# Kernel optimization log

Hardware: AMD Instinct MI355X
Metric: run time of the kernel (lower is better)

Reference implementation:

```python
import jax, jax.numpy as jnp
import numpy as np

N, E, L, H, C, F_IN = 50000, 800000, 3, 8, 16, 128  # nodes, edges, layers, heads, per-head dim, input dim
NEG_SLOPE = 0.2


def setup_inputs() -> dict:
    key = jax.random.key(0)
    k = jax.random.split(key, 8)
    scale = 0.1
    x = jax.random.normal(k[0], (N, F_IN), dtype=jnp.float32)
    Ws = jax.random.normal(k[1], (L, F_IN, H * C), dtype=jnp.float32) * scale
    att_src = jax.random.normal(k[2], (L, H, C), dtype=jnp.float32) * scale
    att_dst = jax.random.normal(k[3], (L, H, C), dtype=jnp.float32) * scale
    biases = jnp.zeros((L, H * C), dtype=jnp.float32)
    fc_w = jax.random.normal(k[4], (H * C, C), dtype=jnp.float32) * scale
    fc_b = jnp.zeros((C,), dtype=jnp.float32)
    edge_index = jax.random.randint(k[5], (2, E), 0, N, dtype=jnp.int64)
    return {"x": x, "Ws": Ws, "att_src": att_src, "att_dst": att_dst,
            "biases": biases, "fc_w": fc_w, "fc_b": fc_b, "edge_index": edge_index}


def _gat_layer(x, W, a_src, a_dst, b, src, dst):
    # x: [N, F]; W: [F, H*C]; a_src/a_dst: [H, C]; src/dst: [E+N] (self-loops included)
    n = x.shape[0]
    h = (x @ W).reshape(n, H, C)                      # [N, H, C]
    e_src = jnp.einsum('nhc,hc->nh', h, a_src)        # [N, H]
    e_dst = jnp.einsum('nhc,hc->nh', h, a_dst)
    e = jax.nn.leaky_relu(e_src[src] + e_dst[dst], NEG_SLOPE)   # [E+N, H]
    # segment softmax over incoming edges of each target node
    emax = jax.ops.segment_max(e, dst, num_segments=n)          # [N, H]
    ex = jnp.exp(e - emax[dst])
    denom = jax.ops.segment_sum(ex, dst, num_segments=n)        # [N, H]
    alpha = ex / (denom[dst] + 1e-16)                            # [E+N, H]
    out = jax.ops.segment_sum(alpha[:, :, None] * h[src], dst, num_segments=n)  # [N, H, C]
    return out.reshape(n, H * C) + b


def reference(x, Ws, att_src, att_dst, biases, fc_w, fc_b, edge_index):
    loop = jnp.arange(N, dtype=edge_index.dtype)
    src = jnp.concatenate([edge_index[0], loop])  # add self-loops (PyG default)
    dst = jnp.concatenate([edge_index[1], loop])
    h = x
    for l in range(L):
        h = _gat_layer(h, Ws[l], att_src[l], att_dst[l], biases[l], src, dst)
        h = jax.nn.elu(h)
    return h @ fc_w + fc_b  # [N, C]
```

## Files before the change

kernel.cpp:

```cpp
#include <hip/hip_runtime.h>
#include <hip/hip_bf16.h>


#define GAT_F 128
#define GAT_H 8
#define GAT_C 16

typedef __attribute__((ext_vector_type(8))) short bf16x8;
typedef __attribute__((ext_vector_type(4))) float f32x4;

__device__ __forceinline__ float bf2f(unsigned short u) {
    union { unsigned int i; float f; } x; x.i = ((unsigned int)u) << 16; return x.f;
}
__device__ __forceinline__ float bfhi2f(unsigned int u) {
    union { unsigned int i; float f; } x; x.i = u & 0xFFFF0000u; return x.f;
}
__device__ __forceinline__ float bflo2f(unsigned int u) {
    union { unsigned int i; float f; } x; x.i = u << 16; return x.f;
}
__device__ __forceinline__ unsigned int pk_bf16(float a, float b) {
    union { float f; unsigned int i; } ua, ub;
    ua.f = a; ub.f = b;
    unsigned int ra = (ua.i + 0x7FFFu + ((ua.i >> 16) & 1u)) >> 16;
    unsigned int rb = (ub.i + 0x7FFFu + ((ub.i >> 16) & 1u)) & 0xFFFF0000u;
    return ra | rb;
}
__device__ __forceinline__ unsigned short f2bf(float a) {
    union { float f; unsigned int i; } ua; ua.f = a;
    return (unsigned short)((ua.i + 0x7FFFu + ((ua.i >> 16) & 1u)) >> 16);
}
__device__ __forceinline__ float ldf(const void* p, size_t i, int isf32) {
    return isf32 ? ((const float*)p)[i] : bf2f(((const unsigned short*)p)[i]);
}
__device__ __forceinline__ int ldei(const int* ei, int i, int is64) {
    return is64 ? ei[2 * (size_t)i] : ei[i];
}

__global__ void k_detect(const unsigned short* __restrict__ xb,
                         const int* __restrict__ ei, int* flags) {
    __shared__ int nan_cnt, zero_cnt;
    if (threadIdx.x == 0) { nan_cnt = 0; zero_cnt = 0; }
    __syncthreads();
    int t = threadIdx.x;
    int ln = 0;
    for (int i = t; i < 8192; i += 256) {
        unsigned short u = xb[i];
        if ((u & 0x7F80) == 0x7F80) ln++;
    }
    int lz = 0;
    for (int i = t; i < 2048; i += 256) {
        if (ei[2 * i + 1] == 0) lz++;
    }
    if (ln) atomicAdd(&nan_cnt, ln);
    if (lz) atomicAdd(&zero_cnt, lz);
    __syncthreads();
    if (t == 0) {
        flags[0] = (nan_cnt > 3) ? 1 : 0;
        flags[1] = (zero_cnt > 1024) ? 1 : 0;
    }
}

__global__ void k_prep(const void* __restrict__ W, const void* __restrict__ asrc,
                       const void* __restrict__ adst,
                       unsigned short* __restrict__ wt, unsigned short* __restrict__ wa,
                       int Lw, const int* __restrict__ flags) {
    int isf32 = flags[0];
    int b = blockIdx.x, t = threadIdx.x;
    if (b < Lw * 64) {
        int gid = b * 256 + t;
        int l = gid >> 14, r = gid & 16383;
        int c = r >> 7, k = r & 127;
        float v = ldf(W, (size_t)l * 16384 + k * 128 + c, isf32);
        wt[gid] = f2bf(v);
    } else {
        int id = (b - Lw * 64) * 256 + t;
        int l = id >> 11, q = id & 2047;
        int j = q >> 7, k = q & 127;
        int head = j & 7;
        const void* av = (j < 8) ? asrc : adst;
        float acc = 0.f;
        #pragma unroll
        for (int cc = 0; cc < 16; cc++) {
            float w = ldf(W, (size_t)l * 16384 + k * 128 + head * 16 + cc, isf32);
            float a = ldf(av, (size_t)l * 128 + head * 16 + cc, isf32);
            acc += w * a;
        }
        wa[id] = f2bf(acc);
    }
}

__global__ void k_init_deg(int* deg, int n) {
    int i = blockIdx.x * 256 + threadIdx.x;
    if (i < n) deg[i] = 1;
}

__global__ void k_count_deg(const int* __restrict__ ei, int* deg, int E,
                            const int* __restrict__ flags) {
    int k = blockIdx.x * 256 + threadIdx.x;
    int is64 = flags[1];
    if (k < E) atomicAdd(&deg[ldei(ei, E + k, is64)], 1);
}

__global__ __launch_bounds__(256) void k_scan_blk(
    const int* __restrict__ deg, int* __restrict__ rp_local,
    int* __restrict__ bsum, int n)
{
    int b = blockIdx.x, t = threadIdx.x;
    int i0 = b * 1024 + t * 4;
    int v0 = 0, v1 = 0, v2 = 0, v3 = 0;
    if (i0 + 3 < n) {
        int4 d = *(const int4*)(deg + i0);
        v0 = d.x; v1 = d.y; v2 = d.z; v3 = d.w;
    } else {
        if (i0     < n) v0 = deg[i0];
        if (i0 + 1 < n) v1 = deg[i0 + 1];
        if (i0 + 2 < n) v2 = deg[i0 + 2];
        if (i0 + 3 < n) v3 = deg[i0 + 3];
    }
    int s = v0 + v1 + v2 + v3;
    int lane = t & 63, wid = t >> 6;
    int sc = s;
    #pragma unroll
    for (int off = 1; off < 64; off <<= 1) {
        int o = __shfl_up(sc, off);
        if (lane >= off) sc += o;
    }
    __shared__ int wsum[4];
    if (lane == 63) wsum[wid] = sc;
    __syncthreads();
    int woff = 0;
    #pragma unroll
    for (int w2 = 0; w2 < 4; w2++) if (w2 < wid) woff += wsum[w2];
    int excl = woff + sc - s;
    if (i0     < n) rp_local[i0]     = excl;
    if (i0 + 1 < n) rp_local[i0 + 1] = excl + v0;
    if (i0 + 2 < n) rp_local[i0 + 2] = excl + v0 + v1;
    if (i0 + 3 < n) rp_local[i0 + 3] = excl + v0 + v1 + v2;
    if (t == 255) bsum[b] = woff + sc;
}

__global__ __launch_bounds__(256) void k_scan_top(
    int* __restrict__ bsum, int* __restrict__ rowptr, int nb, int n)
{
    __shared__ int sh[1024];
    int t = threadIdx.x;
    for (int i = t; i < 1024; i += 256) sh[i] = (i < nb) ? bsum[i] : 0;
    __syncthreads();
    for (int off = 1; off < 1024; off <<= 1) {
        int vals[4];
        #pragma unroll
        for (int k = 0; k < 4; k++) {
            int i = t + 256 * k;
            vals[k] = (i >= off) ? sh[i - off] : 0;
        }
        __syncthreads();
        #pragma unroll
        for (int k = 0; k < 4; k++) sh[t + 256 * k] += vals[k];
        __syncthreads();
    }
    for (int i = t; i < nb; i += 256) bsum[i] = (i == 0) ? 0 : sh[i - 1];
    if (t == 0) rowptr[n] = sh[nb - 1];
}

__global__ void k_place_add(int* __restrict__ rowptr, const int* __restrict__ bsum,
                            int* __restrict__ adj, int* __restrict__ cursor, int n)
{
    int i = blockIdx.x * 256 + threadIdx.x;
    if (i < n) {
        int r = rowptr[i] + bsum[i >> 10];
        rowptr[i] = r;
        adj[r] = i;
        cursor[i] = 1;
    }
    if (blockIdx.x == 0 && threadIdx.x < 8) adj[rowptr[n] + threadIdx.x] = 0;
}

__global__ void k_scatter(const int* __restrict__ ei, const int* __restrict__ rowptr,
                          int* __restrict__ cursor, int* __restrict__ adj, int E,
                          const int* __restrict__ flags) {
    int k = blockIdx.x * 256 + threadIdx.x;
    int is64 = flags[1];
    if (k < E) {
        int s = ldei(ei, k, is64);
        int d = ldei(ei, E + k, is64);
        int p = atomicAdd(&cursor[d], 1);
        adj[rowptr[d] + p] = s;
    }
}

__global__ __launch_bounds__(256) void k_gemm_mfma(
    const void* __restrict__ xin, int x_is_input,
    const unsigned short* __restrict__ wt,
    const unsigned short* __restrict__ wa,
    unsigned int* __restrict__ hb, float* __restrict__ es, float* __restrict__ ed,
    int n, const int* __restrict__ flags)
{
    __shared__ unsigned short xl[64 * 136];
    __shared__ unsigned short wl[144 * 136];
    int isf32 = flags[0];
    int t = threadIdx.x;
    int row0 = blockIdx.x * 64;

    if (isf32 || !x_is_input) {
        const float4* xg = (const float4*)xin;
        for (int i = t; i < 2048; i += 256) {
            int r = i >> 5, c4 = i & 31;
            int gr = row0 + r;
            uint2 u = make_uint2(0u, 0u);
            if (gr < n) {
                float4 v = xg[(size_t)gr * 32 + c4];
                u = make_uint2(pk_bf16(v.x, v.y), pk_bf16(v.z, v.w));
            }
            *(uint2*)&xl[r * 136 + c4 * 4] = u;
        }
    } else {
        const ushort4* xg = (const ushort4*)xin;
        for (int i = t; i < 2048; i += 256) {
            int r = i >> 5, c4 = i & 31;
            int gr = row0 + r;
            ushort4 v = make_ushort4(0, 0, 0, 0);
            if (gr < n) v = xg[(size_t)gr * 32 + c4];
            *(ushort4*)&xl[r * 136 + c4 * 4] = v;
        }
    }
    {
        const ushort4* wg = (const ushort4*)wt;
        for (int i = t; i < 4096; i += 256) {
            int c = i >> 5, k4 = i & 31;
            *(ushort4*)&wl[c * 136 + k4 * 4] = wg[i];
        }
        const ushort4* wag = (const ushort4*)wa;
        for (int i = t; i < 512; i += 256) {
            int j = i >> 5, k4 = i & 31;
            *(ushort4*)&wl[(128 + j) * 136 + k4 * 4] = wag[i];
        }
    }
    __syncthreads();

    int lane = t & 63, wid = t >> 6, quad = lane >> 4, col = lane & 15;
    f32x4 acc[9];
    #pragma unroll
    for (int ct = 0; ct < 9; ct++) acc[ct] = (f32x4){0.f, 0.f, 0.f, 0.f};

    #pragma unroll
    for (int ks = 0; ks < 4; ks++) {
        int k0 = ks * 32;
        bf16x8 af = *(const bf16x8*)&xl[(wid * 16 + col) * 136 + k0 + quad * 8];
        #pragma unroll
        for (int ct = 0; ct < 9; ct++) {
            bf16x8 bf = *(const bf16x8*)&wl[(ct * 16 + col) * 136 + k0 + quad * 8];
            acc[ct] = __builtin_amdgcn_mfma_f32_16x16x32_bf16(af, bf, acc[ct], 0, 0, 0);
        }
    }

    #pragma unroll
    for (int ct = 0; ct < 8; ct++) {
        #pragma unroll
        for (int r = 0; r < 4; r++) {
            int grow = row0 + wid * 16 + quad * 4 + r;
            float v = acc[ct][r];
            float vp = __shfl_xor(v, 1);
            if (!(lane & 1) && grow < n)
                hb[(size_t)grow * 64 + ct * 8 + (col >> 1)] = pk_bf16(v, vp);
        }
    }
    #pragma unroll
    for (int r = 0; r < 4; r++) {
        int grow = row0 + wid * 16 + quad * 4 + r;
        float v = acc[8][r];
        if (grow < n) {
            if (col < 8) es[(size_t)grow * 8 + col] = v;
            else         ed[(size_t)grow * 8 + col - 8] = v;
        }
    }
}

__global__ __launch_bounds__(256) void k_aggregate(
    const unsigned int* __restrict__ hb,
    const float* __restrict__ es, const float* __restrict__ ed,
    const int* __restrict__ rowptr, const int* __restrict__ adj,
    const void* __restrict__ bias, long b_off, float* __restrict__ out, int n,
    const int* __restrict__ flags)
{
    __shared__ __align__(16) float alds[4][64 * 12];
    __shared__ __align__(16) int   slds[4][64];
    int isf32 = flags[0];
    int lane = threadIdx.x & 63;
    int wid = threadIdx.x >> 6;
    int node = blockIdx.x * 4 + wid;
    if (node >= n) return;
    int base = rowptr[node];
    int deg = rowptr[node + 1] - base;
    int head = lane >> 3;

    const float4* es4 = (const float4*)es;
    const float4* ed4 = (const float4*)ed;
    float edv[8];
    {
        float4 a = ed4[node * 2];
        float4 b = ed4[node * 2 + 1];
        edv[0] = a.x; edv[1] = a.y; edv[2] = a.z; edv[3] = a.w;
        edv[4] = b.x; edv[5] = b.y; edv[6] = b.z; edv[7] = b.w;
    }

    float acc0 = 0.f, acc1 = 0.f, lsum = 0.f;
    for (int j0 = 0; j0 < deg; j0 += 64) {
        int j = j0 + lane;
        int sp = (j < deg) ? adj[base + j] : 0;
        float4 ea = es4[sp * 2];
        float4 eb = es4[sp * 2 + 1];
        float ev[8] = {ea.x, ea.y, ea.z, ea.w, eb.x, eb.y, eb.z, eb.w};
        float p[8];
        #pragma unroll
        for (int hh = 0; hh < 8; hh++) {
            float v = ev[hh] + edv[hh];
            v = fmaxf(v, 0.2f * v);
            float pe = __expf(v);
            p[hh] = (j < deg) ? pe : 0.f;
        }
        *(float4*)&alds[wid][lane * 12]     = make_float4(p[0], p[1], p[2], p[3]);
        *(float4*)&alds[wid][lane * 12 + 4] = make_float4(p[4], p[5], p[6], p[7]);
        slds[wid][lane] = sp;
        __builtin_amdgcn_s_waitcnt(0);

        int lim = min(64, deg - j0);
        for (int jj = 0; jj < lim; jj += 4) {
            int4 sv = *(const int4*)&slds[wid][jj];
            float a0 = alds[wid][(jj + 0) * 12 + head];
            float a1 = alds[wid][(jj + 1) * 12 + head];
            float a2 = alds[wid][(jj + 2) * 12 + head];
            float a3 = alds[wid][(jj + 3) * 12 + head];
            unsigned int h0 = hb[sv.x * 64 + lane];
            unsigned int h1 = hb[sv.y * 64 + lane];
            unsigned int h2 = hb[sv.z * 64 + lane];
            unsigned int h3 = hb[sv.w * 64 + lane];
            lsum += (a0 + a1) + (a2 + a3);
            acc0 += a0 * bflo2f(h0) + a1 * bflo2f(h1) + a2 * bflo2f(h2) + a3 * bflo2f(h3);
            acc1 += a0 * bfhi2f(h0) + a1 * bfhi2f(h1) + a2 * bfhi2f(h2) + a3 * bfhi2f(h3);
        }
    }

    float inv = 1.f / (lsum + 1e-16f);
    int ch = lane << 1;
    float o0 = acc0 * inv + ldf(bias, b_off + ch, isf32);
    float o1 = acc1 * inv + ldf(bias, b_off + ch + 1, isf32);
    o0 = o0 > 0.f ? o0 : (__expf(o0) - 1.f);
    o1 = o1 > 0.f ? o1 : (__expf(o1) - 1.f);
    *(float2*)(out + (size_t)node * GAT_F + ch) = make_float2(o0, o1);
}

__global__ __launch_bounds__(256) void k_fc(
    const float* __restrict__ h, const void* __restrict__ fw,
    const void* __restrict__ fb, void* __restrict__ out, int n,
    const int* __restrict__ flags)
{
    __shared__ float fws[GAT_F * GAT_C];
    int isf32 = flags[0];
    int t = threadIdx.x;
    for (int i = t; i < GAT_F * GAT_C; i += 256)
        fws[i] = ldf(fw, i, isf32);
    __syncthreads();
    int row = blockIdx.x * 256 + t;
    if (row >= n) return;
    float acc[16];
    #pragma unroll
    for (int c = 0; c < 16; c++) acc[c] = ldf(fb, c, isf32);
    const float4* hr = (const float4*)(h + (size_t)row * GAT_F);
    for (int k4 = 0; k4 < GAT_F / 4; k4++) {
        float4 xv = hr[k4];
        float xs4[4] = {xv.x, xv.y, xv.z, xv.w};
        #pragma unroll
        for (int kk = 0; kk < 4; kk++) {
            int k = k4 * 4 + kk;
            const float4* wr = (const float4*)(fws + k * GAT_C);
            #pragma unroll
            for (int c4 = 0; c4 < 4; c4++) {
                float4 wv = wr[c4];
                acc[c4 * 4 + 0] += xs4[kk] * wv.x;
                acc[c4 * 4 + 1] += xs4[kk] * wv.y;
                acc[c4 * 4 + 2] += xs4[kk] * wv.z;
                acc[c4 * 4 + 3] += xs4[kk] * wv.w;
            }
        }
    }
    if (isf32) {
        float* o = (float*)out + (size_t)row * GAT_C;
        #pragma unroll
        for (int c = 0; c < 16; c++) o[c] = acc[c];
    } else {
        __hip_bfloat16* o = (__hip_bfloat16*)out + (size_t)row * GAT_C;
        #pragma unroll
        for (int c = 0; c < 16; c++) o[c] = __float2bfloat16(acc[c]);
    }
}

extern "C" void kernel_launch(void* const* d_in, const int* in_sizes, int n_in,
                              void* d_out, int out_size, void* d_ws, size_t ws_size,
                              hipStream_t stream) {
    const void* x      = d_in[0];
    const void* Ws     = d_in[1];
    const void* att_s  = d_in[2];
    const void* att_d  = d_in[3];
    const void* biases = d_in[4];
    const void* fc_w   = d_in[5];
    const void* fc_b   = d_in[6];
    const int*  ei     = (const int*)d_in[7];

    const int N  = in_sizes[0] / GAT_F;
    const int E  = in_sizes[7] / 2;
    const int L  = in_sizes[1] / (GAT_F * GAT_F);
    const int ET = E + N;

    char* w = (char*)d_ws;
    int* flags         = (int*)w;            w += 64;
    float* hA          = (float*)w;          w += (size_t)N * GAT_F * 4;
    unsigned int* hB   = (unsigned int*)w;   w += (size_t)N * 64 * 4;
    float* es          = (float*)w;          w += (size_t)N * GAT_H * 4;
    float* ed          = (float*)w;          w += (size_t)N * GAT_H * 4;
    int* rowptr        = (int*)w;            w += (((size_t)(N + 1) * 4 + 15) & ~15ull);
    int* cursor        = (int*)w;            w += (size_t)N * 4;
    int* bsum          = (int*)w;            w += 1024 * 4;
    int* adj           = (int*)w;            w += (size_t)(ET + 16) * 4;
    unsigned short* wt = (unsigned short*)w; w += (size_t)L * 16384 * 2;
    unsigned short* wa = (unsigned short*)w; w += (size_t)L * 2048 * 2;

    int nb_n = (N + 255) / 256;
    int nb_e = (E + 255) / 256;
    int nb_s = (N + 1023) / 1024;

    k_detect<<<1, 256, 0, stream>>>((const unsigned short*)x, ei, flags);
    k_prep<<<L * 64 + L * 8, 256, 0, stream>>>(Ws, att_s, att_d, wt, wa, L, flags);

    k_init_deg<<<nb_n, 256, 0, stream>>>(cursor, N);
    k_count_deg<<<nb_e, 256, 0, stream>>>(ei, cursor, E, flags);
    k_scan_blk<<<nb_s, 256, 0, stream>>>(cursor, rowptr, bsum, N);
    k_scan_top<<<1, 256, 0, stream>>>(bsum, rowptr, nb_s, N);
    k_place_add<<<nb_n, 256, 0, stream>>>(rowptr, bsum, adj, cursor, N);
    k_scatter<<<nb_e, 256, 0, stream>>>(ei, rowptr, cursor, adj, E, flags);

    int nb_g = (N + 63) / 64;
    int nb_a = (N + 3) / 4;
    for (int l = 0; l < L; l++) {
        k_gemm_mfma<<<nb_g, 256, 0, stream>>>(
            (l == 0) ? x : (const void*)hA, (l == 0) ? 1 : 0,
            wt + (size_t)l * 16384, wa + (size_t)l * 2048,
            hB, es, ed, N, flags);
        k_aggregate<<<nb_a, 256, 0, stream>>>(
            hB, es, ed, rowptr, adj,
            biases, (long)l * GAT_F, hA, N, flags);
    }
    k_fc<<<nb_n, 256, 0, stream>>>(hA, fc_w, fc_b, d_out, N, flags);
}
```

Before: 400.6 us.

## Store hidden activations as bf16, read GEMM operands directly, unroll aggregation by eight

Intermediate layer outputs are now packed bf16 instead of fp32, which halves the write traffic in aggregate and the read traffic in the following GEMM and FC kernels. The GEMM no longer stages weights in LDS and reads bf16 activations straight from global memory, keeping LDS staging only for the fp32 input. Aggregation gathers eight neighbours per iteration, with padded zero slots and a relaxed waitcnt. Edge count and scatter kernels handle two edges per thread with vector loads. The extra bf16 rounding between layers reduces precision, and the uncached global loads of the B operand may cost more than LDS reads.

```diff
diff --git a/kernel.cpp b/kernel.cpp
--- a/kernel.cpp
+++ b/kernel.cpp
@@ -96,9 +96,17 @@
 
 __global__ void k_count_deg(const int* __restrict__ ei, int* deg, int E,
                             const int* __restrict__ flags) {
-    int k = blockIdx.x * 256 + threadIdx.x;
+    int k2 = (blockIdx.x * 256 + threadIdx.x) * 2;
     int is64 = flags[1];
-    if (k < E) atomicAdd(&deg[ldei(ei, E + k, is64)], 1);
+    if (k2 + 1 < E) {
+        int d0, d1;
+        if (is64) { int4 v = *(const int4*)&ei[2 * (size_t)(E + k2)]; d0 = v.x; d1 = v.z; }
+        else      { int2 v = *(const int2*)&ei[E + k2]; d0 = v.x; d1 = v.y; }
+        atomicAdd(&deg[d0], 1);
+        atomicAdd(&deg[d1], 1);
+    } else if (k2 < E) {
+        atomicAdd(&deg[ldei(ei, E + k2, is64)], 1);
+    }
 }
 
 __global__ __launch_bounds__(256) void k_scan_blk(
@@ -178,11 +186,24 @@
 __global__ void k_scatter(const int* __restrict__ ei, const int* __restrict__ rowptr,
                           int* __restrict__ cursor, int* __restrict__ adj, int E,
                           const int* __restrict__ flags) {
-    int k = blockIdx.x * 256 + threadIdx.x;
+    int k2 = (blockIdx.x * 256 + threadIdx.x) * 2;
     int is64 = flags[1];
-    if (k < E) {
-        int s = ldei(ei, k, is64);
-        int d = ldei(ei, E + k, is64);
+    if (k2 + 1 < E) {
+        int s0, s1, d0, d1;
+        if (is64) {
+            int4 a = *(const int4*)&ei[2 * (size_t)k2];       s0 = a.x; s1 = a.z;
+            int4 b = *(const int4*)&ei[2 * (size_t)(E + k2)]; d0 = b.x; d1 = b.z;
+        } else {
+            int2 a = *(const int2*)&ei[k2];     s0 = a.x; s1 = a.y;
+            int2 b = *(const int2*)&ei[E + k2]; d0 = b.x; d1 = b.y;
+        }
+        int p0 = atomicAdd(&cursor[d0], 1);
+        adj[rowptr[d0] + p0] = s0;
+        int p1 = atomicAdd(&cursor[d1], 1);
+        adj[rowptr[d1] + p1] = s1;
+    } else if (k2 < E) {
+        int s = ldei(ei, k2, is64);
+        int d = ldei(ei, E + k2, is64);
         int p = atomicAdd(&cursor[d], 1);
         adj[rowptr[d] + p] = s;
     }
@@ -196,12 +217,13 @@
     int n, const int* __restrict__ flags)
 {
     __shared__ unsigned short xl[64 * 136];
-    __shared__ unsigned short wl[144 * 136];
     int isf32 = flags[0];
     int t = threadIdx.x;
     int row0 = blockIdx.x * 64;
-
-    if (isf32 || !x_is_input) {
+    int lane = t & 63, wid = t >> 6, quad = lane >> 4, col = lane & 15;
+
+    bool direct = (!x_is_input) || (!isf32);
+    if (!direct) {
         const float4* xg = (const float4*)xin;
         for (int i = t; i < 2048; i += 256) {
             int r = i >> 5, c4 = i & 31;
@@ -213,31 +235,15 @@
             }
             *(uint2*)&xl[r * 136 + c4 * 4] = u;
         }
-    } else {
-        const ushort4* xg = (const ushort4*)xin;
-        for (int i = t; i < 2048; i += 256) {
-            int r = i >> 5, c4 = i & 31;
-            int gr = row0 + r;
-            ushort4 v = make_ushort4(0, 0, 0, 0);
-            if (gr < n) v = xg[(size_t)gr * 32 + c4];
-            *(ushort4*)&xl[r * 136 + c4 * 4] = v;
-        }
-    }
-    {
-        const ushort4* wg = (const ushort4*)wt;
-        for (int i = t; i < 4096; i += 256) {
-            int c = i >> 5, k4 = i & 31;
-            *(ushort4*)&wl[c * 136 + k4 * 4] = wg[i];
-        }
-        const ushort4* wag = (const ushort4*)wa;
-        for (int i = t; i < 512; i += 256) {
-            int j = i >> 5, k4 = i & 31;
-            *(ushort4*)&wl[(128 + j) * 136 + k4 * 4] = wag[i];
-        }
-    }
-    __syncthreads();
-
-    int lane = t & 63, wid = t >> 6, quad = lane >> 4, col = lane & 15;
+        __syncthreads();
+    }
+
+    int arow = row0 + wid * 16 + col;
+    int arowc = min(arow, n - 1);
+    const unsigned short* xrow = direct
+        ? ((const unsigned short*)xin + (size_t)arowc * 128)
+        : &xl[(wid * 16 + col) * 136];
+
     f32x4 acc[9];
     #pragma unroll
     for (int ct = 0; ct < 9; ct++) acc[ct] = (f32x4){0.f, 0.f, 0.f, 0.f};
@@ -245,10 +251,12 @@
     #pragma unroll
     for (int ks = 0; ks < 4; ks++) {
         int k0 = ks * 32;
-        bf16x8 af = *(const bf16x8*)&xl[(wid * 16 + col) * 136 + k0 + quad * 8];
+        bf16x8 af = *(const bf16x8*)&xrow[k0 + quad * 8];
         #pragma unroll
         for (int ct = 0; ct < 9; ct++) {
-            bf16x8 bf = *(const bf16x8*)&wl[(ct * 16 + col) * 136 + k0 + quad * 8];
+            const unsigned short* bsrc = (ct < 8) ? &wt[(ct * 16 + col) * 128]
+                                                  : &wa[col * 128];
+            bf16x8 bf = *(const bf16x8*)&bsrc[k0 + quad * 8];
             acc[ct] = __builtin_amdgcn_mfma_f32_16x16x32_bf16(af, bf, acc[ct], 0, 0, 0);
         }
     }
@@ -279,11 +287,11 @@
     const unsigned int* __restrict__ hb,
     const float* __restrict__ es, const float* __restrict__ ed,
     const int* __restrict__ rowptr, const int* __restrict__ adj,
-    const void* __restrict__ bias, long b_off, float* __restrict__ out, int n,
-    const int* __restrict__ flags)
-{
-    __shared__ __align__(16) float alds[4][64 * 12];
-    __shared__ __align__(16) int   slds[4][64];
+    const void* __restrict__ bias, long b_off, unsigned int* __restrict__ out,
+    int n, const int* __restrict__ flags)
+{
+    __shared__ __align__(16) float alds[4][72 * 12];
+    __shared__ __align__(16) int   slds[4][80];
     int isf32 = flags[0];
     int lane = threadIdx.x & 63;
     int wid = threadIdx.x >> 6;
@@ -293,6 +301,12 @@
     int deg = rowptr[node + 1] - base;
     int head = lane >> 3;
 
+    if (lane < 8) {
+        *(float4*)&alds[wid][(64 + lane) * 12]     = make_float4(0.f, 0.f, 0.f, 0.f);
+        *(float4*)&alds[wid][(64 + lane) * 12 + 4] = make_float4(0.f, 0.f, 0.f, 0.f);
+        slds[wid][64 + lane] = 0;
+    }
+
     const float4* es4 = (const float4*)es;
     const float4* ed4 = (const float4*)ed;
     float edv[8];
@@ -321,22 +335,33 @@
         *(float4*)&alds[wid][lane * 12]     = make_float4(p[0], p[1], p[2], p[3]);
         *(float4*)&alds[wid][lane * 12 + 4] = make_float4(p[4], p[5], p[6], p[7]);
         slds[wid][lane] = sp;
-        __builtin_amdgcn_s_waitcnt(0);
+        __builtin_amdgcn_s_waitcnt(0xC07F);
 
         int lim = min(64, deg - j0);
-        for (int jj = 0; jj < lim; jj += 4) {
-            int4 sv = *(const int4*)&slds[wid][jj];
+        for (int jj = 0; jj < lim; jj += 8) {
+            int4 sA = *(const int4*)&slds[wid][jj];
+            int4 sB = *(const int4*)&slds[wid][jj + 4];
             float a0 = alds[wid][(jj + 0) * 12 + head];
             float a1 = alds[wid][(jj + 1) * 12 + head];
             float a2 = alds[wid][(jj + 2) * 12 + head];
             float a3 = alds[wid][(jj + 3) * 12 + head];
-            unsigned int h0 = hb[sv.x * 64 + lane];
-            unsigned int h1 = hb[sv.y * 64 + lane];
-            unsigned int h2 = hb[sv.z * 64 + lane];
-            unsigned int h3 = hb[sv.w * 64 + lane];
-            lsum += (a0 + a1) + (a2 + a3);
+            float a4 = alds[wid][(jj + 4) * 12 + head];
+            float a5 = alds[wid][(jj + 5) * 12 + head];
+            float a6 = alds[wid][(jj + 6) * 12 + head];
+            float a7 = alds[wid][(jj + 7) * 12 + head];
+            unsigned int h0 = hb[sA.x * 64 + lane];
+            unsigned int h1 = hb[sA.y * 64 + lane];
+            unsigned int h2 = hb[sA.z * 64 + lane];
+            unsigned int h3 = hb[sA.w * 64 + lane];
+            unsigned int h4 = hb[sB.x * 64 + lane];
+            unsigned int h5 = hb[sB.y * 64 + lane];
+            unsigned int h6 = hb[sB.z * 64 + lane];
+            unsigned int h7 = hb[sB.w * 64 + lane];
+            lsum += ((a0 + a1) + (a2 + a3)) + ((a4 + a5) + (a6 + a7));
             acc0 += a0 * bflo2f(h0) + a1 * bflo2f(h1) + a2 * bflo2f(h2) + a3 * bflo2f(h3);
+            acc0 += a4 * bflo2f(h4) + a5 * bflo2f(h5) + a6 * bflo2f(h6) + a7 * bflo2f(h7);
             acc1 += a0 * bfhi2f(h0) + a1 * bfhi2f(h1) + a2 * bfhi2f(h2) + a3 * bfhi2f(h3);
+            acc1 += a4 * bfhi2f(h4) + a5 * bfhi2f(h5) + a6 * bfhi2f(h6) + a7 * bfhi2f(h7);
         }
     }
 
@@ -346,11 +371,11 @@
     float o1 = acc1 * inv + ldf(bias, b_off + ch + 1, isf32);
     o0 = o0 > 0.f ? o0 : (__expf(o0) - 1.f);
     o1 = o1 > 0.f ? o1 : (__expf(o1) - 1.f);
-    *(float2*)(out + (size_t)node * GAT_F + ch) = make_float2(o0, o1);
+    out[(size_t)node * 64 + lane] = pk_bf16(o0, o1);
 }
 
 __global__ __launch_bounds__(256) void k_fc(
-    const float* __restrict__ h, const void* __restrict__ fw,
+    const unsigned int* __restrict__ h, const void* __restrict__ fw,
     const void* __restrict__ fb, void* __restrict__ out, int n,
     const int* __restrict__ flags)
 {
@@ -365,22 +390,19 @@
     float acc[16];
     #pragma unroll
     for (int c = 0; c < 16; c++) acc[c] = ldf(fb, c, isf32);
-    const float4* hr = (const float4*)(h + (size_t)row * GAT_F);
-    for (int k4 = 0; k4 < GAT_F / 4; k4++) {
-        float4 xv = hr[k4];
-        float xs4[4] = {xv.x, xv.y, xv.z, xv.w};
-        #pragma unroll
-        for (int kk = 0; kk < 4; kk++) {
-            int k = k4 * 4 + kk;
-            const float4* wr = (const float4*)(fws + k * GAT_C);
-            #pragma unroll
-            for (int c4 = 0; c4 < 4; c4++) {
-                float4 wv = wr[c4];
-                acc[c4 * 4 + 0] += xs4[kk] * wv.x;
-                acc[c4 * 4 + 1] += xs4[kk] * wv.y;
-                acc[c4 * 4 + 2] += xs4[kk] * wv.z;
-                acc[c4 * 4 + 3] += xs4[kk] * wv.w;
-            }
+    const unsigned int* hr = h + (size_t)row * 64;
+    for (int k2 = 0; k2 < 64; k2++) {
+        unsigned int u = hr[k2];
+        float x0 = bflo2f(u), x1 = bfhi2f(u);
+        const float4* w0 = (const float4*)&fws[(2 * k2) * 16];
+        const float4* w1 = (const float4*)&fws[(2 * k2 + 1) * 16];
+        #pragma unroll
+        for (int c4 = 0; c4 < 4; c4++) {
+            float4 wv0 = w0[c4], wv1 = w1[c4];
+            acc[c4 * 4 + 0] += x0 * wv0.x + x1 * wv1.x;
+            acc[c4 * 4 + 1] += x0 * wv0.y + x1 * wv1.y;
+            acc[c4 * 4 + 2] += x0 * wv0.z + x1 * wv1.z;
+            acc[c4 * 4 + 3] += x0 * wv0.w + x1 * wv1.w;
         }
     }
     if (isf32) {
@@ -413,7 +435,7 @@
 
     char* w = (char*)d_ws;
     int* flags         = (int*)w;            w += 64;
-    float* hA          = (float*)w;          w += (size_t)N * GAT_F * 4;
+    unsigned int* hA   = (unsigned int*)w;   w += (size_t)N * 64 * 4;
     unsigned int* hB   = (unsigned int*)w;   w += (size_t)N * 64 * 4;
     float* es          = (float*)w;          w += (size_t)N * GAT_H * 4;
     float* ed          = (float*)w;          w += (size_t)N * GAT_H * 4;
@@ -424,19 +446,19 @@
     unsigned short* wt = (unsigned short*)w; w += (size_t)L * 16384 * 2;
     unsigned short* wa = (unsigned short*)w; w += (size_t)L * 2048 * 2;
 
-    int nb_n = (N + 255) / 256;
-    int nb_e = (E + 255) / 256;
-    int nb_s = (N + 1023) / 1024;
+    int nb_n  = (N + 255) / 256;
+    int nb_e2 = (E + 511) / 512;
+    int nb_s  = (N + 1023) / 1024;
 
     k_detect<<<1, 256, 0, stream>>>((const unsigned short*)x, ei, flags);
     k_prep<<<L * 64 + L * 8, 256, 0, stream>>>(Ws, att_s, att_d, wt, wa, L, flags);
 
     k_init_deg<<<nb_n, 256, 0, stream>>>(cursor, N);
-    k_count_deg<<<nb_e, 256, 0, stream>>>(ei, cursor, E, flags);
+    k_count_deg<<<nb_e2, 256, 0, stream>>>(ei, cursor, E, flags);
     k_scan_blk<<<nb_s, 256, 0, stream>>>(cursor, rowptr, bsum, N);
     k_scan_top<<<1, 256, 0, stream>>>(bsum, rowptr, nb_s, N);
     k_place_add<<<nb_n, 256, 0, stream>>>(rowptr, bsum, adj, cursor, N);
-    k_scatter<<<nb_e, 256, 0, stream>>>(ei, rowptr, cursor, adj, E, flags);
+    k_scatter<<<nb_e2, 256, 0, stream>>>(ei, rowptr, cursor, adj, E, flags);
 
     int nb_g = (N + 63) / 64;
     int nb_a = (N + 3) / 4;
```

Measured after the change: 419.1 us. 1.05x slower.
